# Optimization experiments

Measured on AMD Instinct MI355X. Metric: run time of the kernel, lower is better.

Reference implementation:

```python
import jax, jax.numpy as jnp
import numpy as np

N_HEAD = 8
N_GROUPS = 4
EPS = 1e-5


def setup_inputs() -> dict:
    key = jax.random.key(0)
    ks = jax.random.split(key, 4)
    B, C, D, H, W = 4, 256, 32, 32, 32
    x = jax.random.normal(ks[0], (B, C, D, H, W), dtype=jnp.float32)
    gamma = jnp.ones((C,), dtype=jnp.float32)
    beta = jnp.zeros((C,), dtype=jnp.float32)
    # 1x1 Conv3d == channel matmul; fan-in scaled init
    w_qkv = jax.random.normal(ks[1], (3 * C, C), dtype=jnp.float32) / np.sqrt(C)
    w_out = jax.random.normal(ks[2], (C, C), dtype=jnp.float32) / np.sqrt(C)
    b_out = jnp.zeros((C,), dtype=jnp.float32)
    return {"x": x, "gamma": gamma, "beta": beta, "w_qkv": w_qkv,
            "w_out": w_out, "b_out": b_out}


def _group_norm(x, gamma, beta):
    B, C = x.shape[0], x.shape[1]
    xg = x.reshape(B, N_GROUPS, C // N_GROUPS, *x.shape[2:])
    mu = xg.mean(axis=(2, 3, 4, 5), keepdims=True)
    var = xg.var(axis=(2, 3, 4, 5), keepdims=True)
    xn = ((xg - mu) * jax.lax.rsqrt(var + EPS)).reshape(x.shape)
    return xn * gamma[None, :, None, None, None] + beta[None, :, None, None, None]


def reference(x, gamma, beta, w_qkv, w_out, b_out):
    B, C, D, H, W = x.shape
    n = D * H * W
    dh = C // N_HEAD
    norm = _group_norm(x, gamma, beta)                       # [B,C,D,H,W]
    flat = norm.reshape(B, C, n)                             # [B,C,n]
    qkv = jnp.einsum('oc,bcn->bon', w_qkv, flat)             # [B,3C,n]
    q, k, v = jnp.split(qkv, 3, axis=1)
    q = q.reshape(B, N_HEAD, dh, n)
    k = k.reshape(B, N_HEAD, dh, n)
    v = v.reshape(B, N_HEAD, dh, n)
    k = jax.nn.softmax(k, axis=-1)                           # over tokens n
    q = jax.nn.softmax(q, axis=-2)                           # over head dim d
    context = jnp.einsum('bhdn,bhen->bhde', k, v)            # [B,h,d,d]
    out = jnp.einsum('bhde,bhdn->bhen', context, q)          # [B,h,d,n]
    out = out.reshape(B, C, n)
    out = jnp.einsum('oc,bcn->bon', w_out, out) + b_out[None, :, None]
    return out.reshape(B, C, D, H, W) + x
```

## Files before the change

### kernel.cpp

```cpp
#include <hip/hip_runtime.h>
#include <hip/hip_bf16.h>
#include <math.h>

#define NTOK  32768
#define GNEPS 1e-5f

typedef __attribute__((ext_vector_type(4))) float f32x4;
typedef __attribute__((ext_vector_type(8))) short s16x8;
typedef __attribute__((ext_vector_type(4))) unsigned short u16x4;
typedef __attribute__((ext_vector_type(4))) unsigned int u32x4;

__device__ __forceinline__ unsigned short f2b(float f) {
  unsigned int u = __float_as_uint(f);
  unsigned int r = (u + 0x7FFFu + ((u >> 16) & 1u)) >> 16;
  return (unsigned short)r;
}
__device__ __forceinline__ float b2f(unsigned short s) {
  return __uint_as_float(((unsigned int)s) << 16);
}
__device__ __forceinline__ unsigned char f2f8(float f) {
#if __has_builtin(__builtin_amdgcn_cvt_pk_fp8_f32)
  return (unsigned char)(__builtin_amdgcn_cvt_pk_fp8_f32(f, f, 0, false) & 0xff);
#else
  unsigned int u = __float_as_uint(f);
  unsigned int sgn = (u >> 24) & 0x80;
  float af = fabsf(f);
  if (af > 448.f) return (unsigned char)(sgn | 0x7E);
  if (af < 1e-10f) return (unsigned char)sgn;
  int e; float m = frexpf(af, &e);
  int ee = e + 6;
  if (ee < 1) { m = ldexpf(m, ee - 1); ee = 0; m *= 2.f; }
  int mant = (int)(m * 16.f + 0.5f) - 8;
  if (mant >= 8) { mant = 0; ee += 1; }
  if (mant < 0) mant = 0;
  if (ee > 15) return (unsigned char)(sgn | 0x7E);
  return (unsigned char)(sgn | (ee << 3) | mant);
#endif
}
__device__ __forceinline__ unsigned int pk4f8(float a, float b, float c, float d) {
#if __has_builtin(__builtin_amdgcn_cvt_pk_fp8_f32)
  unsigned int p = (unsigned int)__builtin_amdgcn_cvt_pk_fp8_f32(a, b, 0, false);
  return (unsigned int)__builtin_amdgcn_cvt_pk_fp8_f32(c, d, (int)p, true);
#else
  return (unsigned int)f2f8(a) | ((unsigned int)f2f8(b) << 8)
       | ((unsigned int)f2f8(c) << 16) | ((unsigned int)f2f8(d) << 24);
#endif
}

__device__ __forceinline__ void stage16(const unsigned short* g, unsigned short* ldsChunkBase, int lane) {
#if __has_builtin(__builtin_amdgcn_global_load_lds)
  __builtin_amdgcn_global_load_lds((const __attribute__((address_space(1))) void*)g,
                                   (__attribute__((address_space(3))) void*)ldsChunkBase, 16, 0, 0);
#else
  *(s16x8*)((char*)ldsChunkBase + lane * 16) = *(const s16x8*)g;
#endif
}
__device__ __forceinline__ void stage16b(const unsigned char* g, unsigned char* ldsChunkBase, int lane) {
#if __has_builtin(__builtin_amdgcn_global_load_lds)
  __builtin_amdgcn_global_load_lds((const __attribute__((address_space(1))) void*)g,
                                   (__attribute__((address_space(3))) void*)ldsChunkBase, 16, 0, 0);
#else
  *(f32x4*)(ldsChunkBase + lane * 16) = *(const f32x4*)g;
#endif
}

#define OFF_GSTAT   0u
#define OFF_SSUM    4224u
#define OFF_CTX     8320u
#define OFF_WCTX8   139392u
#define OFF_BIASP   401536u
#define OFF_WP      413824u
#define OFF_XT      1986688u
#define OFF_QT      69095552u
#define OFF_KVB     102649984u
#define WS_NEEDED   (OFF_KVB + 67108864ull)

__global__ __launch_bounds__(256) void gn_fused(const float* __restrict__ x,
                                                float* __restrict__ gstat,
                                                unsigned short* __restrict__ xT) {
  __shared__ unsigned short s1[256 * 64];
  __shared__ float rs[4][4], rq[4][4];
  int b = blockIdx.y;
  int n0 = blockIdx.x * 64;
  int tid = threadIdx.x;
  const float* xb = x + (size_t)b * 256 * NTOK;
  float s[4] = {0.f, 0.f, 0.f, 0.f}, sq[4] = {0.f, 0.f, 0.f, 0.f};
#pragma unroll
  for (int it = 0; it < 16; ++it) {
    int idx = tid + it * 256;
    int c = idx >> 4, q = idx & 15;
    f32x4 v = *reinterpret_cast<const f32x4*>(&xb[(size_t)c * NTOK + n0 + q * 4]);
    const int g = it >> 2;
    s[g]  += v.x + v.y + v.z + v.w;
    sq[g] += v.x * v.x + v.y * v.y + v.z * v.z + v.w * v.w;
    u16x4 o = { f2b(v.x), f2b(v.y), f2b(v.z), f2b(v.w) };
    int phys = (q * 4 + (c >> 3) * 4) & 63;
    *reinterpret_cast<u16x4*>(&s1[c * 64 + phys]) = o;
  }
  int lane = tid & 63, w = tid >> 6;
#pragma unroll
  for (int g = 0; g < 4; ++g) {
    float a = s[g], bq = sq[g];
    for (int o = 32; o > 0; o >>= 1) { a += __shfl_down(a, o); bq += __shfl_down(bq, o); }
    if (lane == 0) { rs[w][g] = a; rq[w][g] = bq; }
  }
  __syncthreads();
  if (tid < 8) {
    int g = tid >> 1, part = tid & 1;
    float v = part ? (rq[0][g] + rq[1][g] + rq[2][g] + rq[3][g])
                   : (rs[0][g] + rs[1][g] + rs[2][g] + rs[3][g]);
    atomicAdd(&gstat[2 * (b * 4 + g) + part], v);
  }
#pragma unroll
  for (int it = 0; it < 8; ++it) {
    int task = tid + it * 256;
    int n = task >> 5, oc = task & 31;
    int phys = (n + oc * 4) & 63;
    s16x8 pk;
#pragma unroll
    for (int i = 0; i < 8; ++i) pk[i] = (short)s1[(oc * 8 + i) * 64 + phys];
    *reinterpret_cast<s16x8*>(&xT[((size_t)(b * NTOK + n0 + n)) * 256 + oc * 8]) = pk;
  }
}

__global__ __launch_bounds__(256) void fold_w(const float* __restrict__ wqkv,
                                              const float* __restrict__ gamma,
                                              const float* __restrict__ beta,
                                              const float* __restrict__ gstat,
                                              unsigned short* __restrict__ Wp,
                                              float* __restrict__ biasp) {
  int o = blockIdx.x, b = blockIdx.y;
  int c = threadIdx.x;
  int g = c >> 6;
  const float cnt = 64.f * (float)NTOK;
  float mu  = gstat[2 * (b * 4 + g)] / cnt;
  float var = gstat[2 * (b * 4 + g) + 1] / cnt - mu * mu;
  float rsig = rsqrtf(var + GNEPS);
  float wv = wqkv[(size_t)o * 256 + c];
  float A = gamma[c] * rsig;
  float Bc = beta[c] - mu * A;
  Wp[((size_t)b * 768 + o) * 256 + c] = f2b(wv * A);
  float t = wv * Bc;
  int lane = c & 63, w = c >> 6;
  for (int off = 32; off > 0; off >>= 1) t += __shfl_down(t, off);
  __shared__ float red[4];
  if (lane == 0) red[w] = t;
  __syncthreads();
  if (c == 0) biasp[b * 768 + o] = red[0] + red[1] + red[2] + red[3];
}

__global__ __launch_bounds__(512, 4) void qkv_gemm(const unsigned short* __restrict__ Wp,
                                                   const float* __restrict__ biasp,
                                                   const unsigned short* __restrict__ xT,
                                                   unsigned char* __restrict__ qT8,
                                                   unsigned char* __restrict__ kvb8) {
  __shared__ unsigned short smem[24576];
  unsigned short* As = smem;
  unsigned short* Bs = smem + 16384;
  int bid = blockIdx.x;
  int L = (bid & 7) * 384 + (bid >> 3);
  int ot = L % 3;
  int t2 = L / 3;
  int b = t2 & 3, nt = t2 >> 2;
  int n0 = nt * 128;
  int tid = threadIdx.x;
  int w = tid >> 6, l = tid & 63;
  int hi = (l >> 4) & 3, lo = l & 15;
  int wo = w >> 1, wn = w & 1;
  int lr = l >> 3, lj = l & 7;
  int srcj = lj ^ lr;
  const unsigned short* Abase = Wp + ((size_t)(b * 768 + ot * 256)) * 256;
  const unsigned short* Bbase = xT + ((size_t)(b * NTOK + n0)) * 256;

  f32x4 acc[4][4];
#pragma unroll
  for (int s = 0; s < 4; ++s)
#pragma unroll
    for (int n = 0; n < 4; ++n) acc[s][n] = (f32x4){0.f, 0.f, 0.f, 0.f};

  for (int c0 = 0; c0 < 256; c0 += 64) {
    __syncthreads();
#pragma unroll
    for (int q = 0; q < 4; ++q) {
      int chunk = w * 4 + q; int row = chunk * 8 + lr;
      stage16(Abase + (size_t)row * 256 + c0 + srcj * 8, As + chunk * 512, l);
    }
#pragma unroll
    for (int q = 0; q < 2; ++q) {
      int chunk = w * 2 + q; int row = chunk * 8 + lr;
      stage16(Bbase + (size_t)row * 256 + c0 + srcj * 8, Bs + chunk * 512, l);
    }
    __syncthreads();
#pragma unroll
    for (int t = 0; t < 2; ++t) {
      s16x8 af[4], bf[4];
#pragma unroll
      for (int s = 0; s < 4; ++s) {
        int row = wo * 64 + s * 16 + lo;
        int phys = (t * 4 + hi) ^ (row & 7);
        af[s] = *reinterpret_cast<const s16x8*>(&As[row * 64 + phys * 8]);
      }
#pragma unroll
      for (int n = 0; n < 4; ++n) {
        int row = wn * 64 + n * 16 + lo;
        int phys = (t * 4 + hi) ^ (row & 7);
        bf[n] = *reinterpret_cast<const s16x8*>(&Bs[row * 64 + phys * 8]);
      }
#pragma unroll
      for (int s = 0; s < 4; ++s)
#pragma unroll
        for (int n = 0; n < 4; ++n)
          acc[s][n] = __builtin_amdgcn_mfma_f32_16x16x32_bf16(af[s], bf[n], acc[s][n], 0, 0, 0);
    }
  }

#pragma unroll
  for (int s = 0; s < 4; ++s)
#pragma unroll
    for (int i = 0; i < 4; ++i) {
      float bv = biasp[b * 768 + ot * 256 + wo * 64 + s * 16 + hi * 4 + i];
#pragma unroll
      for (int n = 0; n < 4; ++n) acc[s][n][i] += bv;
    }

  if (ot == 0) {
    for (int r = 0; r < 2; ++r) {
      __syncthreads();
      if (wn == r) {
#pragma unroll
        for (int s = 0; s < 4; ++s)
#pragma unroll
          for (int n = 0; n < 4; ++n)
#pragma unroll
            for (int i = 0; i < 4; ++i) {
              int o_l = wo * 64 + s * 16 + hi * 4 + i;
              int n_l = n * 16 + lo;
              smem[n_l * 264 + o_l] = f2b(acc[s][n][i]);
            }
      }
      __syncthreads();
      {
        int n_l = tid >> 3, h = tid & 7;
        unsigned short* rowp = &smem[n_l * 264 + h * 32];
        float v[32];
        float m = -1e30f;
#pragma unroll
        for (int i = 0; i < 32; ++i) { v[i] = b2f(rowp[i]); m = fmaxf(m, v[i]); }
        float ssum = 0.f;
#pragma unroll
        for (int i = 0; i < 32; ++i) { v[i] = __expf(v[i] - m); ssum += v[i]; }
        float rr = 1.f / ssum;
#pragma unroll
        for (int i = 0; i < 32; ++i) rowp[i] = f2b(v[i] * rr);
      }
      __syncthreads();
#pragma unroll
      for (int it = 0; it < 2; ++it) {
        int task = tid + it * 512;
        int n_l = task >> 4, j = task & 15;
        const unsigned short* src = &smem[n_l * 264 + j * 16];
        u32x4 pk;
#pragma unroll
        for (int q2 = 0; q2 < 4; ++q2)
          pk[q2] = pk4f8(b2f(src[q2 * 4]), b2f(src[q2 * 4 + 1]),
                         b2f(src[q2 * 4 + 2]), b2f(src[q2 * 4 + 3]));
        *reinterpret_cast<u32x4*>(&qT8[((size_t)(b * NTOK + n0 + r * 64 + n_l)) * 256 + j * 16]) = pk;
      }
    }
  } else {
    unsigned char* smem8 = reinterpret_cast<unsigned char*>(smem);
    int vbase = (ot == 1) ? 0 : 256;
    for (int r = 0; r < 2; ++r) {
      __syncthreads();
      if ((wo >> 1) == r) {
#pragma unroll
        for (int s = 0; s < 4; ++s)
#pragma unroll
          for (int n = 0; n < 4; ++n)
#pragma unroll
            for (int i = 0; i < 4; ++i) {
              int o_l = (wo & 1) * 64 + s * 16 + hi * 4 + i;
              int n_l = wn * 64 + n * 16 + lo;
              float val = acc[s][n][i];
              smem8[o_l * 144 + n_l] = (ot == 1) ? f2f8(__expf(val) * 0.0625f)
                                                 : f2f8(val);
            }
      }
      __syncthreads();
#pragma unroll
      for (int it = 0; it < 2; ++it) {
        int task = tid + it * 512;
        int o_l = task >> 3, j = task & 7;
        f32x4 v = *reinterpret_cast<const f32x4*>(&smem8[o_l * 144 + j * 16]);
        int row = vbase + r * 128 + o_l;
        int local16 = ((n0 & 511) >> 4) + j;
        int phys16 = local16 ^ (row & 7);
        *reinterpret_cast<f32x4*>(&kvb8[((size_t)(b * 512 + row)) * 32768
                                        + (n0 & ~511) + phys16 * 16]) = v;
      }
    }
  }
}

__global__ __launch_bounds__(256) void context_mfma(const unsigned char* __restrict__ kvb8,
                                                    float* __restrict__ ctx,
                                                    float* __restrict__ Ssum) {
  __shared__ unsigned char ctile[32768];
  unsigned char* kl = ctile;
  unsigned char* vl = ctile + 16384;
  int bh = blockIdx.y;
  int b = bh >> 3, h = bh & 7;
  int n0 = blockIdx.x * 512;
  int tid = threadIdx.x;
  int w = tid >> 6, l = tid & 63;
  int lo = l & 15, hi = l >> 4;
  const unsigned char* kb = kvb8 + ((size_t)(b * 512 + h * 32)) * 32768 + n0;
  const unsigned char* vb = kvb8 + ((size_t)(b * 512 + 256 + h * 32)) * 32768 + n0;

#pragma unroll
  for (int q = 0; q < 4; ++q) {
    int chunk = w * 4 + q;
    int row = chunk * 2 + (l >> 5);
    int blk = l & 31;
    stage16b(kb + (size_t)row * 32768 + blk * 16, kl + chunk * 1024, l);
    stage16b(vb + (size_t)row * 32768 + blk * 16, vl + chunk * 1024, l);
  }
  __syncthreads();

  f32x4 acc[2][2], accS[2];
#pragma unroll
  for (int fr = 0; fr < 2; ++fr) {
    accS[fr] = (f32x4){0.f, 0.f, 0.f, 0.f};
#pragma unroll
    for (int fc = 0; fc < 2; ++fc) acc[fr][fc] = (f32x4){0.f, 0.f, 0.f, 0.f};
  }
  long ones = 0x3838383838383838L;

#pragma unroll
  for (int ks = 0; ks < 4; ++ks) {
    int tb = w * 16 + ks * 4 + hi;
    long af[2], bf[2];
#pragma unroll
    for (int fr = 0; fr < 2; ++fr) {
      int row = fr * 16 + lo;
      int off = row * 512 + (((tb >> 1) ^ (row & 7)) << 4) + ((tb & 1) << 3);
      af[fr] = *reinterpret_cast<const long*>(&kl[off]);
      bf[fr] = *reinterpret_cast<const long*>(&vl[off]);
    }
#pragma unroll
    for (int fr = 0; fr < 2; ++fr) {
#pragma unroll
      for (int fc = 0; fc < 2; ++fc)
        acc[fr][fc] = __builtin_amdgcn_mfma_f32_16x16x32_fp8_fp8(af[fr], bf[fc], acc[fr][fc], 0, 0, 0);
      accS[fr] = __builtin_amdgcn_mfma_f32_16x16x32_fp8_fp8(af[fr], ones, accS[fr], 0, 0, 0);
    }
  }
  __syncthreads();

  float* lpart = reinterpret_cast<float*>(ctile);
  float* mine = lpart + w * 1056;
#pragma unroll
  for (int fr = 0; fr < 2; ++fr) {
#pragma unroll
    for (int fc = 0; fc < 2; ++fc)
#pragma unroll
      for (int i = 0; i < 4; ++i) {
        int row = fr * 16 + hi * 4 + i;
        int col = fc * 16 + lo;
        mine[row * 32 + col] = acc[fr][fc][i];
      }
    if (lo == 0)
#pragma unroll
      for (int i = 0; i < 4; ++i)
        mine[1024 + fr * 16 + hi * 4 + i] = accS[fr][i];
  }
  __syncthreads();
  float* cb = ctx + (size_t)bh * 1024;
  for (int i = tid; i < 1024; i += 256) {
    float v = lpart[i] + lpart[1056 + i] + lpart[2112 + i] + lpart[3168 + i];
    atomicAdd(&cb[i], v);
  }
  if (tid < 32) {
    int i = 1024 + tid;
    float v = lpart[i] + lpart[1056 + i] + lpart[2112 + i] + lpart[3168 + i];
    atomicAdd(&Ssum[b * 256 + h * 32 + tid], v);
  }
}

__global__ __launch_bounds__(256) void make_wctx(const float* __restrict__ wout,
                                                 const float* __restrict__ ctx,
                                                 const float* __restrict__ Ssum,
                                                 unsigned char* __restrict__ wctx8) {
  int o = blockIdx.x, b = blockIdx.y;
  int tid = threadIdx.x;
  int h = tid >> 5, d = tid & 31;
  const float* cb = ctx + ((size_t)(b * 8 + h)) * 1024 + d * 32;
  const float* wr = wout + (size_t)o * 256 + h * 32;
  float s = 0.f;
#pragma unroll
  for (int e = 0; e < 32; ++e) s += wr[e] * cb[e];
  s *= (1.f / Ssum[b * 256 + tid]);
  wctx8[((size_t)b * 256 + o) * 256 + tid] = f2f8(s);
}

__global__ __launch_bounds__(512, 4) void out_gemm(const unsigned char* __restrict__ wctx8,
                                                   const unsigned char* __restrict__ qT8,
                                                   const float* __restrict__ bout,
                                                   const float* __restrict__ x,
                                                   float* __restrict__ out) {
  __shared__ unsigned char smem8[49152];
  unsigned char* As = smem8;
  unsigned char* Bs = smem8 + 32768;
  int bid = blockIdx.x;
  int L = (bid & 7) * 128 + (bid >> 3);
  int b = L >> 8, nt = L & 255;
  int n0 = nt * 128;
  int tid = threadIdx.x;
  int w = tid >> 6, l = tid & 63;
  int hi = (l >> 4) & 3, lo = l & 15;
  int wo = w >> 1, wn = w & 1;
  int lr = l >> 3, lj = l & 7;
  int srcj = lj ^ lr;
  const unsigned char* Abase = wctx8 + (size_t)b * 65536;
  const unsigned char* Bbase = qT8 + ((size_t)(b * NTOK + n0)) * 256;

  f32x4 acc[4][4];
#pragma unroll
  for (int s = 0; s < 4; ++s)
#pragma unroll
    for (int n = 0; n < 4; ++n) acc[s][n] = (f32x4){0.f, 0.f, 0.f, 0.f};

  for (int c0 = 0; c0 < 256; c0 += 128) {
    __syncthreads();
#pragma unroll
    for (int q = 0; q < 4; ++q) {
      int chunk = w * 4 + q; int row = chunk * 8 + lr;
      stage16b(Abase + (size_t)row * 256 + c0 + srcj * 16, As + chunk * 1024, l);
    }
#pragma unroll
    for (int q = 0; q < 2; ++q) {
      int chunk = w * 2 + q; int row = chunk * 8 + lr;
      stage16b(Bbase + (size_t)row * 256 + c0 + srcj * 16, Bs + chunk * 1024, l);
    }
    __syncthreads();
#pragma unroll
    for (int t = 0; t < 4; ++t) {
      int blk16 = t * 2 + (hi >> 1);
      int sub8  = (hi & 1) * 8;
      long af[4], bf[4];
#pragma unroll
      for (int s = 0; s < 4; ++s) {
        int row = wo * 64 + s * 16 + lo;
        af[s] = *reinterpret_cast<const long*>(&As[row * 128 + ((blk16 ^ (row & 7)) << 4) + sub8]);
      }
#pragma unroll
      for (int n = 0; n < 4; ++n) {
        int row = wn * 64 + n * 16 + lo;
        bf[n] = *reinterpret_cast<const long*>(&Bs[row * 128 + ((blk16 ^ (row & 7)) << 4) + sub8]);
      }
#pragma unroll
      for (int s = 0; s < 4; ++s)
#pragma unroll
        for (int n = 0; n < 4; ++n)
          acc[s][n] = __builtin_amdgcn_mfma_f32_16x16x32_fp8_fp8(af[s], bf[n], acc[s][n], 0, 0, 0);
    }
  }

  float* bounce = reinterpret_cast<float*>(smem8);
  const float* xb = x + (size_t)b * 256 * NTOK;
  for (int r = 0; r < 4; ++r) {
    __syncthreads();
    if (wo == r) {
#pragma unroll
      for (int s = 0; s < 4; ++s)
#pragma unroll
        for (int n = 0; n < 4; ++n)
#pragma unroll
          for (int i = 0; i < 4; ++i) {
            int o_l = s * 16 + hi * 4 + i;
            int n_l = wn * 64 + n * 16 + lo;
            bounce[o_l * 132 + n_l] = acc[s][n][i];
          }
    }
    __syncthreads();
#pragma unroll
    for (int it = 0; it < 4; ++it) {
      int task = tid + it * 512;
      int o_l = task >> 5, q4 = task & 31;
      int o = r * 64 + o_l;
      f32x4 a = *reinterpret_cast<const f32x4*>(&bounce[o_l * 132 + q4 * 4]);
      f32x4 xv = *reinterpret_cast<const f32x4*>(&xb[(size_t)o * NTOK + n0 + q4 * 4]);
      float bo = bout[o];
      f32x4 rlt = { a.x + bo + xv.x, a.y + bo + xv.y, a.z + bo + xv.z, a.w + bo + xv.w };
      *reinterpret_cast<f32x4*>(&out[((size_t)b * 256 + o) * NTOK + n0 + q4 * 4]) = rlt;
    }
  }
}

extern "C" void kernel_launch(void* const* d_in, const int* in_sizes, int n_in,
                              void* d_out, int out_size, void* d_ws, size_t ws_size,
                              hipStream_t stream) {
  const float* x     = (const float*)d_in[0];
  const float* gamma = (const float*)d_in[1];
  const float* beta  = (const float*)d_in[2];
  const float* wqkv  = (const float*)d_in[3];
  const float* wout  = (const float*)d_in[4];
  const float* bout  = (const float*)d_in[5];
  float* out = (float*)d_out;

  if (ws_size < WS_NEEDED) return;

  char* ws = (char*)d_ws;
  float* gstat        = (float*)(ws + OFF_GSTAT);
  float* Ssum         = (float*)(ws + OFF_SSUM);
  float* ctx          = (float*)(ws + OFF_CTX);
  unsigned char* wctx8 = (unsigned char*)(ws + OFF_WCTX8);
  float* biasp        = (float*)(ws + OFF_BIASP);
  unsigned short* Wp  = (unsigned short*)(ws + OFF_WP);
  unsigned short* xT  = (unsigned short*)(ws + OFF_XT);
  unsigned char* qT8  = (unsigned char*)(ws + OFF_QT);
  unsigned char* kvb8 = (unsigned char*)(ws + OFF_KVB);

  hipMemsetAsync(ws, 0, OFF_CTX + 131072u, stream);

  gn_fused  <<<dim3(512, 4), 256, 0, stream>>>(x, gstat, xT);
  fold_w    <<<dim3(768, 4), 256, 0, stream>>>(wqkv, gamma, beta, gstat, Wp, biasp);
  qkv_gemm  <<<3072, 512, 0, stream>>>(Wp, biasp, xT, qT8, kvb8);
  context_mfma<<<dim3(64, 32), 256, 0, stream>>>(kvb8, ctx, Ssum);
  make_wctx <<<dim3(256, 4), 256, 0, stream>>>(wout, ctx, Ssum, wctx8);
  out_gemm  <<<1024, 512, 0, stream>>>(wctx8, qT8, bout, x, out);
}
```

Measured before the change: 221.4 us.

## Double-buffer LDS staging in QKV GEMM with 32-wide K steps

```diff
diff --git a/kernel.cpp b/kernel.cpp
--- a/kernel.cpp
+++ b/kernel.cpp
@@ -155,8 +155,6 @@
                                                    unsigned char* __restrict__ qT8,
                                                    unsigned char* __restrict__ kvb8) {
   __shared__ unsigned short smem[24576];
-  unsigned short* As = smem;
-  unsigned short* Bs = smem + 16384;
   int bid = blockIdx.x;
   int L = (bid & 7) * 384 + (bid >> 3);
   int ot = L % 3;
@@ -167,8 +165,8 @@
   int w = tid >> 6, l = tid & 63;
   int hi = (l >> 4) & 3, lo = l & 15;
   int wo = w >> 1, wn = w & 1;
-  int lr = l >> 3, lj = l & 7;
-  int srcj = lj ^ lr;
+  int rsw = hi ^ ((lo >> 1) & 3);
+  int srcj = (l & 3) ^ ((l >> 3) & 3);
   const unsigned short* Abase = Wp + ((size_t)(b * 768 + ot * 256)) * 256;
   const unsigned short* Bbase = xT + ((size_t)(b * NTOK + n0)) * 256;
 
@@ -178,40 +176,46 @@
 #pragma unroll
     for (int n = 0; n < 4; ++n) acc[s][n] = (f32x4){0.f, 0.f, 0.f, 0.f};
 
-  for (int c0 = 0; c0 < 256; c0 += 64) {
+  auto stage = [&](int buf, int k0) {
+    unsigned short* As = smem + buf * 12288;
+    unsigned short* Bs = As + 8192;
+#pragma unroll
+    for (int q = 0; q < 2; ++q) {
+      int chunk = w * 2 + q;
+      int row = chunk * 16 + (l >> 2);
+      stage16(Abase + (size_t)row * 256 + k0 + srcj * 8, As + chunk * 512, l);
+    }
+    {
+      int row = w * 16 + (l >> 2);
+      stage16(Bbase + (size_t)row * 256 + k0 + srcj * 8, Bs + w * 512, l);
+    }
+  };
+
+  stage(0, 0);
+  __syncthreads();
+#pragma unroll
+  for (int step = 0; step < 8; ++step) {
+    int cur = step & 1;
+    if (step < 7) stage(cur ^ 1, (step + 1) * 32);
+    const unsigned short* As = smem + cur * 12288;
+    const unsigned short* Bs = As + 8192;
+    s16x8 af[4], bf[4];
+#pragma unroll
+    for (int s = 0; s < 4; ++s) {
+      int row = wo * 64 + s * 16 + lo;
+      af[s] = *reinterpret_cast<const s16x8*>(&As[row * 32 + rsw * 8]);
+    }
+#pragma unroll
+    for (int n = 0; n < 4; ++n) {
+      int row = wn * 64 + n * 16 + lo;
+      bf[n] = *reinterpret_cast<const s16x8*>(&Bs[row * 32 + rsw * 8]);
+    }
+#pragma unroll
+    for (int s = 0; s < 4; ++s)
+#pragma unroll
+      for (int n = 0; n < 4; ++n)
+        acc[s][n] = __builtin_amdgcn_mfma_f32_16x16x32_bf16(af[s], bf[n], acc[s][n], 0, 0, 0);
     __syncthreads();
-#pragma unroll
-    for (int q = 0; q < 4; ++q) {
-      int chunk = w * 4 + q; int row = chunk * 8 + lr;
-      stage16(Abase + (size_t)row * 256 + c0 + srcj * 8, As + chunk * 512, l);
-    }
-#pragma unroll
-    for (int q = 0; q < 2; ++q) {
-      int chunk = w * 2 + q; int row = chunk * 8 + lr;
-      stage16(Bbase + (size_t)row * 256 + c0 + srcj * 8, Bs + chunk * 512, l);
-    }
-    __syncthreads();
-#pragma unroll
-    for (int t = 0; t < 2; ++t) {
-      s16x8 af[4], bf[4];
-#pragma unroll
-      for (int s = 0; s < 4; ++s) {
-        int row = wo * 64 + s * 16 + lo;
-        int phys = (t * 4 + hi) ^ (row & 7);
-        af[s] = *reinterpret_cast<const s16x8*>(&As[row * 64 + phys * 8]);
-      }
-#pragma unroll
-      for (int n = 0; n < 4; ++n) {
-        int row = wn * 64 + n * 16 + lo;
-        int phys = (t * 4 + hi) ^ (row & 7);
-        bf[n] = *reinterpret_cast<const s16x8*>(&Bs[row * 64 + phys * 8]);
-      }
-#pragma unroll
-      for (int s = 0; s < 4; ++s)
-#pragma unroll
-        for (int n = 0; n < 4; ++n)
-          acc[s][n] = __builtin_amdgcn_mfma_f32_16x16x32_bf16(af[s], bf[n], acc[s][n], 0, 0, 0);
-    }
   }
 
 #pragma unroll
```

Measured after the change: 225.0 us. Within noise of the previous version (+1.6%).
